# Kernel tuning notes

Measured on AMD Instinct MI355X. Metric: run time of the kernel, lower is better.

The kernel has to match this reference:

```python
import jax, jax.numpy as jnp
import numpy as np

BATCH, SEQ, D_IN, D_OUT = 32, 1024, 128, 128
NEG_SLOPE = 0.1


def setup_inputs() -> dict:
    key = jax.random.key(0)
    k1, k2, k3, k4 = jax.random.split(key, 4)
    nodes = jax.random.normal(k1, (BATCH, SEQ, D_IN), dtype=jnp.float32)
    adjacent = jax.random.randint(k2, (BATCH, SEQ, SEQ), 0, 2, dtype=jnp.int32)
    W = jax.random.normal(k3, (D_IN, D_OUT), dtype=jnp.float32) / np.sqrt(D_IN)
    B = jax.random.normal(k4, (D_IN, D_OUT), dtype=jnp.float32) / np.sqrt(D_IN)
    return {"nodes": nodes, "adjacent": adjacent, "W": W, "B": B}


def reference(nodes, adjacent, W, B):
    # mask[b, out, in] = 1 if edge (out -> in) present
    mask = (adjacent != 0).astype(nodes.dtype)
    # counts[b, in] = in-degree (number of 'out' neighbors pooled per target node)
    counts = mask.sum(axis=1)                               # [b, s_in]
    # segment-sum of neighbor features: pooled[b, in, d] = sum_out mask * nodes[b, out, d]
    pooled = jnp.einsum('boi,bod->bid', mask, nodes)        # [b, s_in, d]
    # mean over neighbors; nodes with zero degree get no pooled contribution
    pooled = jnp.where(counts[..., None] > 0,
                       pooled / jnp.maximum(counts, 1.0)[..., None],
                       jnp.zeros((), dtype=nodes.dtype))
    updated = nodes @ B + pooled @ W                        # [b, s, d_out]
    return jax.nn.leaky_relu(updated, negative_slope=NEG_SLOPE)
```

## Files before the change

kernel.cpp:

```cpp
#include <hip/hip_runtime.h>
#include <hip/hip_bf16.h>

#define SEQ 1024
#define DIM 128
#define NEG_SLOPE 0.1f

typedef __bf16 bf16x8 __attribute__((ext_vector_type(8)));
typedef float f32x4v __attribute__((ext_vector_type(4)));

#define BUF_STRIDE 24576
#define NODES_OFF  8192

__device__ __forceinline__ int swz(int row, int unit) {
    const int x  = row >> 2;
    const int fx = ((x & 3) | ((x & 1) << 2)) ^ ((x >> 2) & 7);
    return row * 128 + ((unit ^ fx) << 4);
}

__device__ __forceinline__ void bar() {
    asm volatile("s_waitcnt lgkmcnt(0)" ::: "memory");
    __builtin_amdgcn_s_barrier();
    __builtin_amdgcn_sched_barrier(0);
}

__device__ __forceinline__ unsigned short bfb(float f) {
    __bf16 h = (__bf16)f;
    return __builtin_bit_cast(unsigned short, h);
}
__device__ __forceinline__ unsigned mpack(int x0, int x1) {
    unsigned m0 = (x0 != 0) ? 0x3F80u : 0u;
    unsigned m1 = (x1 != 0) ? 0x3F80u : 0u;
    return m0 | (m1 << 16);
}

__global__ __launch_bounds__(256, 2)
void gcn_fused(const float* __restrict__ nodes,
               const int* __restrict__ adj,
               const float* __restrict__ W,
               const float* __restrict__ Bm,
               float* __restrict__ out)
{
    __shared__ alignas(16) unsigned char lds[2 * BUF_STRIDE];

    const int bid   = blockIdx.x;
    const int xcd   = bid & 7;
    const int slot  = bid >> 3;
    const int batch = ((slot >> 4) << 3) | xcd;
    const int mtile = slot & 15;
    const int i0    = mtile << 6;

    const int tid  = threadIdx.x;
    const int wave = tid >> 6;
    const int lane = tid & 63;
    const int wm   = wave >> 1;
    const int wn   = wave & 1;
    const int lrow = lane & 15;
    const int quad = lane >> 4;

    const int*   __restrict__ adj_b   = adj   + (size_t)batch * SEQ * SEQ;
    const float* __restrict__ nodes_b = nodes + (size_t)batch * SEQ * DIM;

    const int a_row = (tid >> 4) * 4;
    const int a_col = (tid & 15) * 4;
    const int n_row = (tid >> 5) * 4;
    const int n_col = (tid & 31) * 4;

    const int m_unit = (tid >> 4) >> 1;
    const int m_sub  = ((tid >> 4) & 1) * 8;
    const int n_unit = (tid >> 5) >> 1;
    const int n_sub  = ((tid >> 5) & 1) * 8;

    f32x4v acc[2][4] = {};
    f32x4v acc_cnt[2] = {};

    bf16x8 ones;
    #pragma unroll
    for (int j = 0; j < 8; ++j) ones[j] = __builtin_bit_cast(__bf16, (unsigned short)0x3F80);

    int4   A0[4], A1[4];
    float4 N0[8], N1[8];

    auto load_chunk = [&](int o0, int4 (&A)[4], float4 (&N)[8]) {
        const int* pa = adj_b + (size_t)(o0 + a_row) * SEQ + (i0 + a_col);
        #pragma unroll
        for (int r = 0; r < 4; ++r) A[r] = *(const int4*)(pa + (size_t)r * SEQ);
        const float* pn = nodes_b + (size_t)(o0 + n_row) * DIM + n_col;
        #pragma unroll
        for (int it = 0; it < 2; ++it)
            #pragma unroll
            for (int r = 0; r < 4; ++r)
                N[it * 4 + r] = *(const float4*)(pn + (size_t)(it * 32 + r) * DIM);
    };

    auto write_lds = [&](int base, const int4 (&A)[4], const float4 (&N)[8]) {
        unsigned char* mb = lds + base;
        unsigned char* nb = lds + base + NODES_OFF;
        #pragma unroll
        for (int j = 0; j < 4; ++j) {
            uint2 w;
            w.x = mpack(((const int*)&A[0])[j], ((const int*)&A[1])[j]);
            w.y = mpack(((const int*)&A[2])[j], ((const int*)&A[3])[j]);
            *(uint2*)(mb + swz(a_col + j, m_unit) + m_sub) = w;
        }
        #pragma unroll
        for (int it = 0; it < 2; ++it) {
            #pragma unroll
            for (int j = 0; j < 4; ++j) {
                uint2 w;
                w.x = (unsigned)bfb(((const float*)&N[it*4+0])[j]) |
                      ((unsigned)bfb(((const float*)&N[it*4+1])[j]) << 16);
                w.y = (unsigned)bfb(((const float*)&N[it*4+2])[j]) |
                      ((unsigned)bfb(((const float*)&N[it*4+3])[j]) << 16);
                *(uint2*)(nb + swz(n_col + j, 4 * it + n_unit) + n_sub) = w;
            }
        }
    };

    auto compute = [&](int base) {
        const unsigned char* mb = lds + base;
        const unsigned char* nb = lds + base + NODES_OFF;
        #pragma unroll
        for (int kk = 0; kk < 2; ++kk) {
            bf16x8 av[2], bv[4];
            av[0] = *(const bf16x8*)(mb + swz(wm * 32 +      lrow, 4 * kk + quad));
            av[1] = *(const bf16x8*)(mb + swz(wm * 32 + 16 + lrow, 4 * kk + quad));
            #pragma unroll
            for (int nf = 0; nf < 4; ++nf)
                bv[nf] = *(const bf16x8*)(nb + swz(wn * 64 + nf * 16 + lrow, 4 * kk + quad));
            #pragma unroll
            for (int mf = 0; mf < 2; ++mf) {
                #pragma unroll
                for (int nf = 0; nf < 4; ++nf)
                    acc[mf][nf] = __builtin_amdgcn_mfma_f32_16x16x32_bf16(av[mf], bv[nf], acc[mf][nf], 0, 0, 0);
                acc_cnt[mf] = __builtin_amdgcn_mfma_f32_16x16x32_bf16(av[mf], ones, acc_cnt[mf], 0, 0, 0);
            }
        }
    };

    load_chunk(0,   A0, N0);
    load_chunk(64,  A1, N1);
    write_lds(0, A0, N0);
    load_chunk(128, A0, N0);
    bar();

    for (int cc = 0; cc < 8; ++cc) {
        const int c0 = cc * 2;
        compute(0);
        write_lds(BUF_STRIDE, A1, N1);
        if (c0 + 3 < 16) load_chunk((c0 + 3) * 64, A1, N1);
        bar();
        compute(BUF_STRIDE);
        if (c0 + 2 < 16) write_lds(0, A0, N0);
        if (c0 + 4 < 16) load_chunk((c0 + 4) * 64, A0, N0);
        bar();
    }

    unsigned short (*pooled)[136] = (unsigned short (*)[136])(void*)lds;
    #pragma unroll
    for (int mf = 0; mf < 2; ++mf) {
        #pragma unroll
        for (int r = 0; r < 4; ++r) {
            const int row = wm * 32 + mf * 16 + quad * 4 + r;
            const float cnt = acc_cnt[mf][r];
            const float inv = (cnt > 0.5f) ? 1.0f / cnt : 0.0f;
            #pragma unroll
            for (int nf = 0; nf < 4; ++nf) {
                const int col = wn * 64 + nf * 16 + lrow;
                pooled[row][col] = bfb(acc[mf][nf][r] * inv);
            }
        }
    }
    __syncthreads();

    f32x4v acc2[2][4] = {};
    const int d_b0 = wn * 64 + lrow;

    #pragma unroll
    for (int ks = 0; ks < 4; ++ks) {
        const int k0 = ks * 32 + quad * 8;
        bf16x8 av[2];
        #pragma unroll
        for (int mf = 0; mf < 2; ++mf)
            av[mf] = *(const bf16x8*)&pooled[wm * 32 + mf * 16 + lrow][k0];
        bf16x8 bv[4];
        const float* pw = W + (size_t)k0 * DIM + d_b0;
        #pragma unroll
        for (int nf = 0; nf < 4; ++nf) {
            #pragma unroll
            for (int j = 0; j < 8; ++j)
                bv[nf][j] = (__bf16)pw[j * DIM + nf * 16];
        }
        #pragma unroll
        for (int mf = 0; mf < 2; ++mf)
            #pragma unroll
            for (int nf = 0; nf < 4; ++nf)
                acc2[mf][nf] = __builtin_amdgcn_mfma_f32_16x16x32_bf16(av[mf], bv[nf], acc2[mf][nf], 0, 0, 0);
    }

    #pragma unroll
    for (int ks = 0; ks < 4; ++ks) {
        const int k0 = ks * 32 + quad * 8;
        bf16x8 av[2];
        #pragma unroll
        for (int mf = 0; mf < 2; ++mf) {
            const float* p = nodes_b + (size_t)(i0 + wm * 32 + mf * 16 + lrow) * DIM + k0;
            const float4 f1 = *(const float4*)p;
            const float4 f2 = *(const float4*)(p + 4);
            av[mf][0] = (__bf16)f1.x; av[mf][1] = (__bf16)f1.y;
            av[mf][2] = (__bf16)f1.z; av[mf][3] = (__bf16)f1.w;
            av[mf][4] = (__bf16)f2.x; av[mf][5] = (__bf16)f2.y;
            av[mf][6] = (__bf16)f2.z; av[mf][7] = (__bf16)f2.w;
        }
        bf16x8 bv[4];
        const float* pB = Bm + (size_t)k0 * DIM + d_b0;
        #pragma unroll
        for (int nf = 0; nf < 4; ++nf) {
            #pragma unroll
            for (int j = 0; j < 8; ++j)
                bv[nf][j] = (__bf16)pB[j * DIM + nf * 16];
        }
        #pragma unroll
        for (int mf = 0; mf < 2; ++mf)
            #pragma unroll
            for (int nf = 0; nf < 4; ++nf)
                acc2[mf][nf] = __builtin_amdgcn_mfma_f32_16x16x32_bf16(av[mf], bv[nf], acc2[mf][nf], 0, 0, 0);
    }

    float* out_b = out + (size_t)batch * SEQ * DIM;
    #pragma unroll
    for (int mf = 0; mf < 2; ++mf) {
        #pragma unroll
        for (int nf = 0; nf < 4; ++nf) {
            const int col = wn * 64 + nf * 16 + lrow;
            #pragma unroll
            for (int r = 0; r < 4; ++r) {
                const int row = i0 + wm * 32 + mf * 16 + quad * 4 + r;
                const float x = acc2[mf][nf][r];
                out_b[(size_t)row * DIM + col] = (x > 0.0f) ? x : NEG_SLOPE * x;
            }
        }
    }
}

extern "C" void kernel_launch(void* const* d_in, const int* in_sizes, int n_in,
                              void* d_out, int out_size, void* d_ws, size_t ws_size,
                              hipStream_t stream) {
    const float* nodes = (const float*)d_in[0];
    const int*   adj   = (const int*)d_in[1];
    const float* W     = (const float*)d_in[2];
    const float* Bm    = (const float*)d_in[3];
    float*       out   = (float*)d_out;
    gcn_fused<<<dim3(512), dim3(256), 0, stream>>>(nodes, adj, W, Bm, out);
}
```

Before: 222.6 us.

## Double block size to 512 threads with 2x4 wave grid and halved per-thread loads

The block grows from 4 to 8 waves over the same 64-row tile. The 2x4 wave grid gives each wave 32 output columns instead of 64, and each thread loads half as much adjacency and node data per chunk. This doubles the number of waves in flight per block to hide the latency of the memory-bound adjacency stream, and lowers per-thread register use. In exchange the ones-MFMA count computation is now done redundantly by twice as many waves, and each block carries more barrier and sync overhead.

After: 228.5 us. 2.7% more time.

```diff
diff --git a/kernel.cpp b/kernel.cpp
--- a/kernel.cpp
+++ b/kernel.cpp
@@ -33,7 +33,7 @@
     return m0 | (m1 << 16);
 }
 
-__global__ __launch_bounds__(256, 2)
+__global__ __launch_bounds__(512, 4)
 void gcn_fused(const float* __restrict__ nodes,
                const int* __restrict__ adj,
                const float* __restrict__ W,
@@ -52,67 +52,58 @@
     const int tid  = threadIdx.x;
     const int wave = tid >> 6;
     const int lane = tid & 63;
-    const int wm   = wave >> 1;
-    const int wn   = wave & 1;
+    const int wm   = wave >> 2;
+    const int wn   = wave & 3;
     const int lrow = lane & 15;
     const int quad = lane >> 4;
 
     const int*   __restrict__ adj_b   = adj   + (size_t)batch * SEQ * SEQ;
     const float* __restrict__ nodes_b = nodes + (size_t)batch * SEQ * DIM;
 
-    const int a_row = (tid >> 4) * 4;
-    const int a_col = (tid & 15) * 4;
-    const int n_row = (tid >> 5) * 4;
-    const int n_col = (tid & 31) * 4;
-
-    const int m_unit = (tid >> 4) >> 1;
-    const int m_sub  = ((tid >> 4) & 1) * 8;
-    const int n_unit = (tid >> 5) >> 1;
-    const int n_sub  = ((tid >> 5) & 1) * 8;
-
-    f32x4v acc[2][4] = {};
+    const int sg     = tid >> 5;
+    const int o_off  = sg * 4;
+    const int a_col2 = (tid & 31) * 2;
+    const int n_col  = (tid & 31) * 4;
+    const int unit_s = sg >> 1;
+    const int sub_s  = (sg & 1) * 8;
+
+    f32x4v acc[2][2] = {};
     f32x4v acc_cnt[2] = {};
 
     bf16x8 ones;
     #pragma unroll
     for (int j = 0; j < 8; ++j) ones[j] = __builtin_bit_cast(__bf16, (unsigned short)0x3F80);
 
-    int4   A0[4], A1[4];
-    float4 N0[8], N1[8];
-
-    auto load_chunk = [&](int o0, int4 (&A)[4], float4 (&N)[8]) {
-        const int* pa = adj_b + (size_t)(o0 + a_row) * SEQ + (i0 + a_col);
-        #pragma unroll
-        for (int r = 0; r < 4; ++r) A[r] = *(const int4*)(pa + (size_t)r * SEQ);
-        const float* pn = nodes_b + (size_t)(o0 + n_row) * DIM + n_col;
-        #pragma unroll
-        for (int it = 0; it < 2; ++it)
-            #pragma unroll
-            for (int r = 0; r < 4; ++r)
-                N[it * 4 + r] = *(const float4*)(pn + (size_t)(it * 32 + r) * DIM);
+    int2   A0[4], A1[4];
+    float4 N0[4], N1[4];
+
+    auto load_chunk = [&](int o0, int2 (&A)[4], float4 (&N)[4]) {
+        const int* pa = adj_b + (size_t)(o0 + o_off) * SEQ + (i0 + a_col2);
+        #pragma unroll
+        for (int r = 0; r < 4; ++r) A[r] = *(const int2*)(pa + (size_t)r * SEQ);
+        const float* pn = nodes_b + (size_t)(o0 + o_off) * DIM + n_col;
+        #pragma unroll
+        for (int r = 0; r < 4; ++r) N[r] = *(const float4*)(pn + (size_t)r * DIM);
     };
 
-    auto write_lds = [&](int base, const int4 (&A)[4], const float4 (&N)[8]) {
+    auto write_lds = [&](int base, const int2 (&A)[4], const float4 (&N)[4]) {
         unsigned char* mb = lds + base;
         unsigned char* nb = lds + base + NODES_OFF;
         #pragma unroll
+        for (int j = 0; j < 2; ++j) {
+            uint2 w;
+            w.x = mpack(j ? A[0].y : A[0].x, j ? A[1].y : A[1].x);
+            w.y = mpack(j ? A[2].y : A[2].x, j ? A[3].y : A[3].x);
+            *(uint2*)(mb + swz(a_col2 + j, unit_s) + sub_s) = w;
+        }
+        #pragma unroll
         for (int j = 0; j < 4; ++j) {
             uint2 w;
-            w.x = mpack(((const int*)&A[0])[j], ((const int*)&A[1])[j]);
-            w.y = mpack(((const int*)&A[2])[j], ((const int*)&A[3])[j]);
-            *(uint2*)(mb + swz(a_col + j, m_unit) + m_sub) = w;
-        }
-        #pragma unroll
-        for (int it = 0; it < 2; ++it) {
-            #pragma unroll
-            for (int j = 0; j < 4; ++j) {
-                uint2 w;
-                w.x = (unsigned)bfb(((const float*)&N[it*4+0])[j]) |
-                      ((unsigned)bfb(((const float*)&N[it*4+1])[j]) << 16);
-                w.y = (unsigned)bfb(((const float*)&N[it*4+2])[j]) |
-                      ((unsigned)bfb(((const float*)&N[it*4+3])[j]) << 16);
-                *(uint2*)(nb + swz(n_col + j, 4 * it + n_unit) + n_sub) = w;
-            }
+            w.x = (unsigned)bfb(((const float*)&N[0])[j]) |
+                  ((unsigned)bfb(((const float*)&N[1])[j]) << 16);
+            w.y = (unsigned)bfb(((const float*)&N[2])[j]) |
+                  ((unsigned)bfb(((const float*)&N[3])[j]) << 16);
+            *(uint2*)(nb + swz(n_col + j, unit_s) + sub_s) = w;
         }
     };
 
@@ -121,16 +112,17 @@
         const unsigned char* nb = lds + base + NODES_OFF;
         #pragma unroll
         for (int kk = 0; kk < 2; ++kk) {
-            bf16x8 av[2], bv[4];
-            av[0] = *(const bf16x8*)(mb + swz(wm * 32 +      lrow, 4 * kk + quad));
-            av[1] = *(const bf16x8*)(mb + swz(wm * 32 + 16 + lrow, 4 * kk + quad));
-            #pragma unroll
-            for (int nf = 0; nf < 4; ++nf)
-                bv[nf] = *(const bf16x8*)(nb + swz(wn * 64 + nf * 16 + lrow, 4 * kk + quad));
+            bf16x8 av[2], bv[2];
+            #pragma unroll
+            for (int mf = 0; mf < 2; ++mf)
+                av[mf] = *(const bf16x8*)(mb + swz(wm * 32 + mf * 16 + lrow, 4 * kk + quad));
+            #pragma unroll
+            for (int nf = 0; nf < 2; ++nf)
+                bv[nf] = *(const bf16x8*)(nb + swz(wn * 32 + nf * 16 + lrow, 4 * kk + quad));
             #pragma unroll
             for (int mf = 0; mf < 2; ++mf) {
                 #pragma unroll
-                for (int nf = 0; nf < 4; ++nf)
+                for (int nf = 0; nf < 2; ++nf)
                     acc[mf][nf] = __builtin_amdgcn_mfma_f32_16x16x32_bf16(av[mf], bv[nf], acc[mf][nf], 0, 0, 0);
                 acc_cnt[mf] = __builtin_amdgcn_mfma_f32_16x16x32_bf16(av[mf], ones, acc_cnt[mf], 0, 0, 0);
             }
@@ -164,16 +156,16 @@
             const float cnt = acc_cnt[mf][r];
             const float inv = (cnt > 0.5f) ? 1.0f / cnt : 0.0f;
             #pragma unroll
-            for (int nf = 0; nf < 4; ++nf) {
-                const int col = wn * 64 + nf * 16 + lrow;
+            for (int nf = 0; nf < 2; ++nf) {
+                const int col = wn * 32 + nf * 16 + lrow;
                 pooled[row][col] = bfb(acc[mf][nf][r] * inv);
             }
         }
     }
     __syncthreads();
 
-    f32x4v acc2[2][4] = {};
-    const int d_b0 = wn * 64 + lrow;
+    f32x4v acc2[2][2] = {};
+    const int d_b0 = wn * 32 + lrow;
 
     #pragma unroll
     for (int ks = 0; ks < 4; ++ks) {
@@ -182,10 +174,10 @@
         #pragma unroll
         for (int mf = 0; mf < 2; ++mf)
             av[mf] = *(const bf16x8*)&pooled[wm * 32 + mf * 16 + lrow][k0];
-        bf16x8 bv[4];
+        bf16x8 bv[2];
         const float* pw = W + (size_t)k0 * DIM + d_b0;
         #pragma unroll
-        for (int nf = 0; nf < 4; ++nf) {
+        for (int nf = 0; nf < 2; ++nf) {
             #pragma unroll
             for (int j = 0; j < 8; ++j)
                 bv[nf][j] = (__bf16)pw[j * DIM + nf * 16];
@@ -193,7 +185,7 @@
         #pragma unroll
         for (int mf = 0; mf < 2; ++mf)
             #pragma unroll
-            for (int nf = 0; nf < 4; ++nf)
+            for (int nf = 0; nf < 2; ++nf)
                 acc2[mf][nf] = __builtin_amdgcn_mfma_f32_16x16x32_bf16(av[mf], bv[nf], acc2[mf][nf], 0, 0, 0);
     }
 
@@ -211,10 +203,10 @@
             av[mf][4] = (__bf16)f2.x; av[mf][5] = (__bf16)f2.y;
             av[mf][6] = (__bf16)f2.z; av[mf][7] = (__bf16)f2.w;
         }
-        bf16x8 bv[4];
+        bf16x8 bv[2];
         const float* pB = Bm + (size_t)k0 * DIM + d_b0;
         #pragma unroll
-        for (int nf = 0; nf < 4; ++nf) {
+        for (int nf = 0; nf < 2; ++nf) {
             #pragma unroll
             for (int j = 0; j < 8; ++j)
                 bv[nf][j] = (__bf16)pB[j * DIM + nf * 16];
@@ -222,7 +214,7 @@
         #pragma unroll
         for (int mf = 0; mf < 2; ++mf)
             #pragma unroll
-            for (int nf = 0; nf < 4; ++nf)
+            for (int nf = 0; nf < 2; ++nf)
                 acc2[mf][nf] = __builtin_amdgcn_mfma_f32_16x16x32_bf16(av[mf], bv[nf], acc2[mf][nf], 0, 0, 0);
     }
 
@@ -230,8 +222,8 @@
     #pragma unroll
     for (int mf = 0; mf < 2; ++mf) {
         #pragma unroll
-        for (int nf = 0; nf < 4; ++nf) {
-            const int col = wn * 64 + nf * 16 + lrow;
+        for (int nf = 0; nf < 2; ++nf) {
+            const int col = wn * 32 + nf * 16 + lrow;
             #pragma unroll
             for (int r = 0; r < 4; ++r) {
                 const int row = i0 + wm * 32 + mf * 16 + quad * 4 + r;
@@ -250,5 +242,5 @@
     const float* W     = (const float*)d_in[2];
     const float* Bm    = (const float*)d_in[3];
     float*       out   = (float*)d_out;
-    gcn_fused<<<dim3(512), dim3(256), 0, stream>>>(nodes, adj, W, Bm, out);
-}
+    gcn_fused<<<dim3(512), dim3(512), 0, stream>>>(nodes, adj, W, Bm, out);
+}
```

## Pre-transpose nodes and weights to bf16, halve the row tile, double the grid

Applied to the files above, without the earlier changes.

Adds two small pre-pass kernels. One converts W and B to transposed bf16 copies, and one writes a transposed bf16 copy of nodes into the workspace. The main kernel then loads the B operand straight from global memory into registers instead of staging it through LDS. The row tile drops from 64 to 32 rows, which doubles the grid to 1024 blocks, shrinks LDS to the mask buffers only, and raises occupancy to 4 blocks per CU. The cost is two extra launches plus an extra write and read of nodes in bf16. The original kernel is kept as a fallback when the workspace is too small.

Result: slower. 240.3 us (+8.0%).

```diff
diff --git a/kernel.cpp b/kernel.cpp
--- a/kernel.cpp
+++ b/kernel.cpp
@@ -8,78 +8,274 @@
 typedef __bf16 bf16x8 __attribute__((ext_vector_type(8)));
 typedef float f32x4v __attribute__((ext_vector_type(4)));
 
-#define BUF_STRIDE 24576
-#define NODES_OFF  8192
-
-__device__ __forceinline__ int swz(int row, int unit) {
-    const int x  = row >> 2;
-    const int fx = ((x & 3) | ((x & 1) << 2)) ^ ((x >> 2) & 7);
-    return row * 128 + ((unit ^ fx) << 4);
-}
-
+__device__ __forceinline__ unsigned short bfb(float f) {
+    __bf16 h = (__bf16)f;
+    return __builtin_bit_cast(unsigned short, h);
+}
+__device__ __forceinline__ unsigned mpack(int x0, int x1) {
+    unsigned m0 = (x0 != 0) ? 0x3F80u : 0u;
+    unsigned m1 = (x1 != 0) ? 0x3F80u : 0u;
+    return m0 | (m1 << 16);
+}
+__device__ __forceinline__ int fxv(int x) {
+    return ((x & 3) | ((x & 1) << 2)) ^ ((x >> 2) & 7);
+}
 __device__ __forceinline__ void bar() {
     asm volatile("s_waitcnt lgkmcnt(0)" ::: "memory");
     __builtin_amdgcn_s_barrier();
     __builtin_amdgcn_sched_barrier(0);
 }
 
-__device__ __forceinline__ unsigned short bfb(float f) {
-    __bf16 h = (__bf16)f;
-    return __builtin_bit_cast(unsigned short, h);
-}
-__device__ __forceinline__ unsigned mpack(int x0, int x1) {
-    unsigned m0 = (x0 != 0) ? 0x3F80u : 0u;
-    unsigned m1 = (x1 != 0) ? 0x3F80u : 0u;
-    return m0 | (m1 << 16);
-}
-
-__global__ __launch_bounds__(256, 2)
+__global__ __launch_bounds__(256)
+void wb_t(const float* __restrict__ W, const float* __restrict__ Bm,
+          unsigned short* __restrict__ WT, unsigned short* __restrict__ BT) {
+    const int gid = blockIdx.x * 256 + threadIdx.x;
+    const int n = gid >> 7, k = gid & 127;
+    WT[gid] = bfb(W[k * DIM + n]);
+    BT[gid] = bfb(Bm[k * DIM + n]);
+}
+
+__global__ __launch_bounds__(256)
+void nodes_t_kernel(const float* __restrict__ nodes, unsigned short* __restrict__ nodesT) {
+    const int b  = blockIdx.x >> 4;
+    const int o0 = (blockIdx.x & 15) << 6;
+    __shared__ unsigned short T[DIM][66];
+
+    const float* src = nodes + (size_t)b * SEQ * DIM;
+    const int t = threadIdx.x & 31;
+    const int g = threadIdx.x >> 5;
+
+    float4 v[8];
+    #pragma unroll
+    for (int r = 0; r < 8; ++r)
+        v[r] = *(const float4*)(src + (size_t)(o0 + g * 8 + r) * DIM + 4 * t);
+    #pragma unroll
+    for (int j = 0; j < 4; ++j) {
+        #pragma unroll
+        for (int p = 0; p < 4; ++p) {
+            unsigned w = (unsigned)bfb(((const float*)&v[2 * p])[j]) |
+                         ((unsigned)bfb(((const float*)&v[2 * p + 1])[j]) << 16);
+            *(unsigned*)((unsigned char*)&T[0][0] + (size_t)(4 * t + j) * 132 + (g * 8 + 2 * p) * 2) = w;
+        }
+    }
+    __syncthreads();
+    const int d = threadIdx.x >> 1, h = threadIdx.x & 1;
+    unsigned u[16];
+    #pragma unroll
+    for (int s = 0; s < 16; ++s)
+        u[s] = *(const unsigned*)((const unsigned char*)&T[0][0] + (size_t)d * 132 + h * 64 + s * 4);
+    unsigned short* dst = nodesT + (size_t)b * DIM * SEQ + (size_t)d * SEQ + o0 + h * 32;
+    #pragma unroll
+    for (int s = 0; s < 4; ++s) {
+        uint4 q = make_uint4(u[4 * s], u[4 * s + 1], u[4 * s + 2], u[4 * s + 3]);
+        *(uint4*)((unsigned char*)dst + s * 16) = q;
+    }
+}
+
+__global__ __launch_bounds__(256, 4)
 void gcn_fused(const float* __restrict__ nodes,
                const int* __restrict__ adj,
-               const float* __restrict__ W,
-               const float* __restrict__ Bm,
+               const unsigned short* __restrict__ nodesT,
+               const unsigned short* __restrict__ WT,
+               const unsigned short* __restrict__ BT,
                float* __restrict__ out)
 {
-    __shared__ alignas(16) unsigned char lds[2 * BUF_STRIDE];
+    __shared__ union {
+        unsigned char  m[2][4096];
+        unsigned short pooled[32][136];
+    } u;
 
     const int bid   = blockIdx.x;
     const int xcd   = bid & 7;
     const int slot  = bid >> 3;
-    const int batch = ((slot >> 4) << 3) | xcd;
-    const int mtile = slot & 15;
-    const int i0    = mtile << 6;
+    const int batch = ((slot >> 5) << 3) | xcd;
+    const int itile = slot & 31;
+    const int i0    = itile << 5;
 
     const int tid  = threadIdx.x;
     const int wave = tid >> 6;
     const int lane = tid & 63;
-    const int wm   = wave >> 1;
-    const int wn   = wave & 1;
     const int lrow = lane & 15;
     const int quad = lane >> 4;
 
-    const int*   __restrict__ adj_b   = adj   + (size_t)batch * SEQ * SEQ;
+    const int*            __restrict__ adj_b   = adj    + (size_t)batch * SEQ * SEQ;
+    const float*          __restrict__ nodes_b = nodes  + (size_t)batch * SEQ * DIM;
+    const unsigned short* __restrict__ nT_b    = nodesT + (size_t)batch * DIM * SEQ;
+
+    const int tq   = tid >> 3;
+    const int ic   = tid & 7;
+    const int fxic = fxv(ic);
+    const int gi0  = i0 + 4 * ic;
+    const int o0   = 2 * tq;
+
+    const int fx0 = fxv(lrow >> 2);
+    const int fx1 = fxv(4 + (lrow >> 2));
+
+    f32x4v acc[2][2] = {};
+    f32x4v acc_cnt[2] = {};
+    bf16x8 ones;
+    #pragma unroll
+    for (int j = 0; j < 8; ++j) ones[j] = __builtin_bit_cast(__bf16, (unsigned short)0x3F80);
+
+    int4   A0[2], A1[2];
+    bf16x8 bvA[4], bvB[4];
+
+    auto load_adj = [&](int c, int4 (&A)[2]) {
+        const int* pa = adj_b + (size_t)(c * 64 + o0) * SEQ + gi0;
+        A[0] = *(const int4*)pa;
+        A[1] = *(const int4*)(pa + SEQ);
+    };
+    auto load_bv = [&](int c, bf16x8 (&bv)[4]) {
+        const unsigned short* pn = nT_b + (size_t)(wave * 32 + lrow) * SEQ + c * 64 + quad * 8;
+        bv[0] = *(const bf16x8*)(pn);
+        bv[1] = *(const bf16x8*)(pn + 16 * SEQ);
+        bv[2] = *(const bf16x8*)(pn + 32);
+        bv[3] = *(const bf16x8*)(pn + 16 * SEQ + 32);
+    };
+    auto write_mask = [&](int b, const int4 (&A)[2]) {
+        unsigned char* mb = u.m[b];
+        #pragma unroll
+        for (int j = 0; j < 4; ++j) {
+            unsigned w = mpack(((const int*)&A[0])[j], ((const int*)&A[1])[j]);
+            *(unsigned*)(mb + (4 * ic + j) * 128 + (((tq >> 2) ^ fxic) << 4) + 4 * (tq & 3)) = w;
+        }
+    };
+    auto compute = [&](int b, const bf16x8 (&bv)[4]) {
+        const unsigned char* mb = u.m[b];
+        #pragma unroll
+        for (int kk = 0; kk < 2; ++kk) {
+            bf16x8 av0 = *(const bf16x8*)(mb + lrow * 128        + (((4 * kk + quad) ^ fx0) << 4));
+            bf16x8 av1 = *(const bf16x8*)(mb + (16 + lrow) * 128 + (((4 * kk + quad) ^ fx1) << 4));
+            acc[0][0] = __builtin_amdgcn_mfma_f32_16x16x32_bf16(av0, bv[2 * kk + 0], acc[0][0], 0, 0, 0);
+            acc[0][1] = __builtin_amdgcn_mfma_f32_16x16x32_bf16(av0, bv[2 * kk + 1], acc[0][1], 0, 0, 0);
+            acc[1][0] = __builtin_amdgcn_mfma_f32_16x16x32_bf16(av1, bv[2 * kk + 0], acc[1][0], 0, 0, 0);
+            acc[1][1] = __builtin_amdgcn_mfma_f32_16x16x32_bf16(av1, bv[2 * kk + 1], acc[1][1], 0, 0, 0);
+            acc_cnt[0] = __builtin_amdgcn_mfma_f32_16x16x32_bf16(av0, ones, acc_cnt[0], 0, 0, 0);
+            acc_cnt[1] = __builtin_amdgcn_mfma_f32_16x16x32_bf16(av1, ones, acc_cnt[1], 0, 0, 0);
+        }
+    };
+
+    load_adj(0, A0); load_adj(1, A1);
+    load_bv(0, bvA); load_bv(1, bvB);
+    write_mask(0, A0);
+    load_adj(2, A0);
+    bar();
+
+    for (int cc = 0; cc < 8; ++cc) {
+        const int c0 = 2 * cc;
+        compute(0, bvA);
+        write_mask(1, A1);
+        if (c0 + 3 < 16) load_adj(c0 + 3, A1);
+        if (c0 + 2 < 16) load_bv(c0 + 2, bvA);
+        bar();
+        compute(1, bvB);
+        if (c0 + 2 < 16) write_mask(0, A0);
+        if (c0 + 4 < 16) load_adj(c0 + 4, A0);
+        if (c0 + 3 < 16) load_bv(c0 + 3, bvB);
+        bar();
+    }
+
+    #pragma unroll
+    for (int mf = 0; mf < 2; ++mf) {
+        #pragma unroll
+        for (int r = 0; r < 4; ++r) {
+            const int row = mf * 16 + quad * 4 + r;
+            const float cnt = acc_cnt[mf][r];
+            const float inv = (cnt > 0.5f) ? 1.0f / cnt : 0.0f;
+            #pragma unroll
+            for (int nf = 0; nf < 2; ++nf)
+                u.pooled[row][wave * 32 + nf * 16 + lrow] = bfb(acc[mf][nf][r] * inv);
+        }
+    }
+    bar();
+
+    f32x4v acc2[2][2] = {};
+    const int dn = wave * 32 + lrow;
+
+    #pragma unroll
+    for (int ks = 0; ks < 4; ++ks) {
+        const int k0 = ks * 32 + quad * 8;
+        bf16x8 av[2], bv2[2];
+        #pragma unroll
+        for (int mf = 0; mf < 2; ++mf)
+            av[mf] = *(const bf16x8*)((const unsigned char*)&u.pooled[0][0] + (mf * 16 + lrow) * 272 + k0 * 2);
+        #pragma unroll
+        for (int nf = 0; nf < 2; ++nf)
+            bv2[nf] = *(const bf16x8*)(WT + (size_t)(dn + nf * 16) * DIM + k0);
+        #pragma unroll
+        for (int mf = 0; mf < 2; ++mf)
+            #pragma unroll
+            for (int nf = 0; nf < 2; ++nf)
+                acc2[mf][nf] = __builtin_amdgcn_mfma_f32_16x16x32_bf16(av[mf], bv2[nf], acc2[mf][nf], 0, 0, 0);
+    }
+    #pragma unroll
+    for (int ks = 0; ks < 4; ++ks) {
+        const int k0 = ks * 32 + quad * 8;
+        bf16x8 av[2], bv2[2];
+        #pragma unroll
+        for (int mf = 0; mf < 2; ++mf) {
+            const float* p = nodes_b + (size_t)(i0 + mf * 16 + lrow) * DIM + k0;
+            const float4 f1 = *(const float4*)p;
+            const float4 f2 = *(const float4*)(p + 4);
+            av[mf][0] = (__bf16)f1.x; av[mf][1] = (__bf16)f1.y;
+            av[mf][2] = (__bf16)f1.z; av[mf][3] = (__bf16)f1.w;
+            av[mf][4] = (__bf16)f2.x; av[mf][5] = (__bf16)f2.y;
+            av[mf][6] = (__bf16)f2.z; av[mf][7] = (__bf16)f2.w;
+        }
+        #pragma unroll
+        for (int nf = 0; nf < 2; ++nf)
+            bv2[nf] = *(const bf16x8*)(BT + (size_t)(dn + nf * 16) * DIM + k0);
+        #pragma unroll
+        for (int mf = 0; mf < 2; ++mf)
+            #pragma unroll
+            for (int nf = 0; nf < 2; ++nf)
+                acc2[mf][nf] = __builtin_amdgcn_mfma_f32_16x16x32_bf16(av[mf], bv2[nf], acc2[mf][nf], 0, 0, 0);
+    }
+
+    float* out_b = out + (size_t)batch * SEQ * DIM;
+    #pragma unroll
+    for (int mf = 0; mf < 2; ++mf) {
+        #pragma unroll
+        for (int nf = 0; nf < 2; ++nf) {
+            const int col = wave * 32 + nf * 16 + lrow;
+            #pragma unroll
+            for (int r = 0; r < 4; ++r) {
+                const int row = i0 + mf * 16 + quad * 4 + r;
+                const float x = acc2[mf][nf][r];
+                out_b[(size_t)row * DIM + col] = (x > 0.0f) ? x : NEG_SLOPE * x;
+            }
+        }
+    }
+}
+
+#define BUF_STRIDE 24576
+#define NODES_OFF  8192
+__device__ __forceinline__ int fb_swz(int row, int unit) {
+    const int x  = row >> 2;
+    const int fx = ((x & 3) | ((x & 1) << 2)) ^ ((x >> 2) & 7);
+    return row * 128 + ((unit ^ fx) << 4);
+}
+__global__ __launch_bounds__(256, 2)
+void gcn_fused_fb(const float* __restrict__ nodes, const int* __restrict__ adj,
+                  const float* __restrict__ W, const float* __restrict__ Bm,
+                  float* __restrict__ out)
+{
+    __shared__ alignas(16) unsigned char lds[2 * BUF_STRIDE];
+    const int bid = blockIdx.x, xcd = bid & 7, slot = bid >> 3;
+    const int batch = ((slot >> 4) << 3) | xcd, mtile = slot & 15, i0 = mtile << 6;
+    const int tid = threadIdx.x, wave = tid >> 6, lane = tid & 63;
+    const int wm = wave >> 1, wn = wave & 1, lrow = lane & 15, quad = lane >> 4;
+    const int* __restrict__ adj_b = adj + (size_t)batch * SEQ * SEQ;
     const float* __restrict__ nodes_b = nodes + (size_t)batch * SEQ * DIM;
-
-    const int a_row = (tid >> 4) * 4;
-    const int a_col = (tid & 15) * 4;
-    const int n_row = (tid >> 5) * 4;
-    const int n_col = (tid & 31) * 4;
-
-    const int m_unit = (tid >> 4) >> 1;
-    const int m_sub  = ((tid >> 4) & 1) * 8;
-    const int n_unit = (tid >> 5) >> 1;
-    const int n_sub  = ((tid >> 5) & 1) * 8;
-
-    f32x4v acc[2][4] = {};
-    f32x4v acc_cnt[2] = {};
-
+    const int a_row = (tid >> 4) * 4, a_col = (tid & 15) * 4;
+    const int n_row = (tid >> 5) * 4, n_col = (tid & 31) * 4;
+    const int m_unit = (tid >> 4) >> 1, m_sub = ((tid >> 4) & 1) * 8;
+    const int n_unit = (tid >> 5) >> 1, n_sub = ((tid >> 5) & 1) * 8;
+    f32x4v acc[2][4] = {}; f32x4v acc_cnt[2] = {};
     bf16x8 ones;
     #pragma unroll
     for (int j = 0; j < 8; ++j) ones[j] = __builtin_bit_cast(__bf16, (unsigned short)0x3F80);
-
-    int4   A0[4], A1[4];
-    float4 N0[8], N1[8];
-
+    int4 A0[4], A1[4]; float4 N0[8], N1[8];
     auto load_chunk = [&](int o0, int4 (&A)[4], float4 (&N)[8]) {
         const int* pa = adj_b + (size_t)(o0 + a_row) * SEQ + (i0 + a_col);
         #pragma unroll
@@ -91,42 +287,36 @@
             for (int r = 0; r < 4; ++r)
                 N[it * 4 + r] = *(const float4*)(pn + (size_t)(it * 32 + r) * DIM);
     };
-
     auto write_lds = [&](int base, const int4 (&A)[4], const float4 (&N)[8]) {
-        unsigned char* mb = lds + base;
-        unsigned char* nb = lds + base + NODES_OFF;
+        unsigned char* mb = lds + base; unsigned char* nb = lds + base + NODES_OFF;
         #pragma unroll
         for (int j = 0; j < 4; ++j) {
             uint2 w;
             w.x = mpack(((const int*)&A[0])[j], ((const int*)&A[1])[j]);
             w.y = mpack(((const int*)&A[2])[j], ((const int*)&A[3])[j]);
-            *(uint2*)(mb + swz(a_col + j, m_unit) + m_sub) = w;
+            *(uint2*)(mb + fb_swz(a_col + j, m_unit) + m_sub) = w;
         }
         #pragma unroll
         for (int it = 0; it < 2; ++it) {
             #pragma unroll
             for (int j = 0; j < 4; ++j) {
                 uint2 w;
-                w.x = (unsigned)bfb(((const float*)&N[it*4+0])[j]) |
-                      ((unsigned)bfb(((const float*)&N[it*4+1])[j]) << 16);
-                w.y = (unsigned)bfb(((const float*)&N[it*4+2])[j]) |
-                      ((unsigned)bfb(((const float*)&N[it*4+3])[j]) << 16);
-                *(uint2*)(nb + swz(n_col + j, 4 * it + n_unit) + n_sub) = w;
+                w.x = (unsigned)bfb(((const float*)&N[it*4+0])[j]) | ((unsigned)bfb(((const float*)&N[it*4+1])[j]) << 16);
+                w.y = (unsigned)bfb(((const float*)&N[it*4+2])[j]) | ((unsigned)bfb(((const float*)&N[it*4+3])[j]) << 16);
+                *(uint2*)(nb + fb_swz(n_col + j, 4 * it + n_unit) + n_sub) = w;
             }
         }
     };
-
     auto compute = [&](int base) {
-        const unsigned char* mb = lds + base;
-        const unsigned char* nb = lds + base + NODES_OFF;
+        const unsigned char* mb = lds + base; const unsigned char* nb = lds + base + NODES_OFF;
         #pragma unroll
         for (int kk = 0; kk < 2; ++kk) {
             bf16x8 av[2], bv[4];
-            av[0] = *(const bf16x8*)(mb + swz(wm * 32 +      lrow, 4 * kk + quad));
-            av[1] = *(const bf16x8*)(mb + swz(wm * 32 + 16 + lrow, 4 * kk + quad));
+            av[0] = *(const bf16x8*)(mb + fb_swz(wm * 32 + lrow, 4 * kk + quad));
+            av[1] = *(const bf16x8*)(mb + fb_swz(wm * 32 + 16 + lrow, 4 * kk + quad));
             #pragma unroll
             for (int nf = 0; nf < 4; ++nf)
-                bv[nf] = *(const bf16x8*)(nb + swz(wn * 64 + nf * 16 + lrow, 4 * kk + quad));
+                bv[nf] = *(const bf16x8*)(nb + fb_swz(wn * 64 + nf * 16 + lrow, 4 * kk + quad));
             #pragma unroll
             for (int mf = 0; mf < 2; ++mf) {
                 #pragma unroll
@@ -136,17 +326,11 @@
             }
         }
     };
-
-    load_chunk(0,   A0, N0);
-    load_chunk(64,  A1, N1);
-    write_lds(0, A0, N0);
-    load_chunk(128, A0, N0);
-    bar();
-
+    load_chunk(0, A0, N0); load_chunk(64, A1, N1);
+    write_lds(0, A0, N0); load_chunk(128, A0, N0); bar();
     for (int cc = 0; cc < 8; ++cc) {
         const int c0 = cc * 2;
-        compute(0);
-        write_lds(BUF_STRIDE, A1, N1);
+        compute(0); write_lds(BUF_STRIDE, A1, N1);
         if (c0 + 3 < 16) load_chunk((c0 + 3) * 64, A1, N1);
         bar();
         compute(BUF_STRIDE);
@@ -154,27 +338,21 @@
         if (c0 + 4 < 16) load_chunk((c0 + 4) * 64, A0, N0);
         bar();
     }
-
     unsigned short (*pooled)[136] = (unsigned short (*)[136])(void*)lds;
     #pragma unroll
-    for (int mf = 0; mf < 2; ++mf) {
+    for (int mf = 0; mf < 2; ++mf)
         #pragma unroll
         for (int r = 0; r < 4; ++r) {
             const int row = wm * 32 + mf * 16 + quad * 4 + r;
             const float cnt = acc_cnt[mf][r];
             const float inv = (cnt > 0.5f) ? 1.0f / cnt : 0.0f;
             #pragma unroll
-            for (int nf = 0; nf < 4; ++nf) {
-                const int col = wn * 64 + nf * 16 + lrow;
-                pooled[row][col] = bfb(acc[mf][nf][r] * inv);
-            }
-        }
-    }
+            for (int nf = 0; nf < 4; ++nf)
+                pooled[row][wn * 64 + nf * 16 + lrow] = bfb(acc[mf][nf][r] * inv);
+        }
     __syncthreads();
-
     f32x4v acc2[2][4] = {};
     const int d_b0 = wn * 64 + lrow;
-
     #pragma unroll
     for (int ks = 0; ks < 4; ++ks) {
         const int k0 = ks * 32 + quad * 8;
@@ -185,18 +363,15 @@
         bf16x8 bv[4];
         const float* pw = W + (size_t)k0 * DIM + d_b0;
         #pragma unroll
-        for (int nf = 0; nf < 4; ++nf) {
-            #pragma unroll
-            for (int j = 0; j < 8; ++j)
-                bv[nf][j] = (__bf16)pw[j * DIM + nf * 16];
-        }
+        for (int nf = 0; nf < 4; ++nf)
+            #pragma unroll
+            for (int j = 0; j < 8; ++j) bv[nf][j] = (__bf16)pw[j * DIM + nf * 16];
         #pragma unroll
         for (int mf = 0; mf < 2; ++mf)
             #pragma unroll
             for (int nf = 0; nf < 4; ++nf)
                 acc2[mf][nf] = __builtin_amdgcn_mfma_f32_16x16x32_bf16(av[mf], bv[nf], acc2[mf][nf], 0, 0, 0);
     }
-
     #pragma unroll
     for (int ks = 0; ks < 4; ++ks) {
         const int k0 = ks * 32 + quad * 8;
@@ -204,8 +379,7 @@
         #pragma unroll
         for (int mf = 0; mf < 2; ++mf) {
             const float* p = nodes_b + (size_t)(i0 + wm * 32 + mf * 16 + lrow) * DIM + k0;
-            const float4 f1 = *(const float4*)p;
-            const float4 f2 = *(const float4*)(p + 4);
+            const float4 f1 = *(const float4*)p; const float4 f2 = *(const float4*)(p + 4);
             av[mf][0] = (__bf16)f1.x; av[mf][1] = (__bf16)f1.y;
             av[mf][2] = (__bf16)f1.z; av[mf][3] = (__bf16)f1.w;
             av[mf][4] = (__bf16)f2.x; av[mf][5] = (__bf16)f2.y;
@@ -214,21 +388,18 @@
         bf16x8 bv[4];
         const float* pB = Bm + (size_t)k0 * DIM + d_b0;
         #pragma unroll
-        for (int nf = 0; nf < 4; ++nf) {
-            #pragma unroll
-            for (int j = 0; j < 8; ++j)
-                bv[nf][j] = (__bf16)pB[j * DIM + nf * 16];
-        }
+        for (int nf = 0; nf < 4; ++nf)
+            #pragma unroll
+            for (int j = 0; j < 8; ++j) bv[nf][j] = (__bf16)pB[j * DIM + nf * 16];
         #pragma unroll
         for (int mf = 0; mf < 2; ++mf)
             #pragma unroll
             for (int nf = 0; nf < 4; ++nf)
                 acc2[mf][nf] = __builtin_amdgcn_mfma_f32_16x16x32_bf16(av[mf], bv[nf], acc2[mf][nf], 0, 0, 0);
     }
-
     float* out_b = out + (size_t)batch * SEQ * DIM;
     #pragma unroll
-    for (int mf = 0; mf < 2; ++mf) {
+    for (int mf = 0; mf < 2; ++mf)
         #pragma unroll
         for (int nf = 0; nf < 4; ++nf) {
             const int col = wn * 64 + nf * 16 + lrow;
@@ -239,7 +410,6 @@
                 out_b[(size_t)row * DIM + col] = (x > 0.0f) ? x : NEG_SLOPE * x;
             }
         }
-    }
 }
 
 extern "C" void kernel_launch(void* const* d_in, const int* in_sizes, int n_in,
@@ -250,5 +420,19 @@
     const float* W     = (const float*)d_in[2];
     const float* Bm    = (const float*)d_in[3];
     float*       out   = (float*)d_out;
-    gcn_fused<<<dim3(512), dim3(256), 0, stream>>>(nodes, adj, W, Bm, out);
-}
+
+    const size_t NT_BYTES = (size_t)32 * DIM * SEQ * 2;
+    const size_t WB_BYTES = (size_t)DIM * DIM * 2;
+    const size_t NEED = NT_BYTES + 2 * WB_BYTES;
+
+    if (d_ws != nullptr && ws_size >= NEED) {
+        unsigned short* nodesT = (unsigned short*)d_ws;
+        unsigned short* WT = (unsigned short*)((char*)d_ws + NT_BYTES);
+        unsigned short* BT = (unsigned short*)((char*)d_ws + NT_BYTES + WB_BYTES);
+        wb_t<<<dim3(64), dim3(256), 0, stream>>>(W, Bm, WT, BT);
+        nodes_t_kernel<<<dim3(512), dim3(256), 0, stream>>>(nodes, nodesT);
+        gcn_fused<<<dim3(1024), dim3(256), 0, stream>>>(nodes, adj, nodesT, WT, BT, out);
+    } else {
+        gcn_fused_fb<<<dim3(512), dim3(256), 0, stream>>>(nodes, adj, W, Bm, out);
+    }
+}
```

## Double output-row tile to 128 per block with 512 threads

Applied to the files above, without the earlier changes.

Each block now covers 128 target rows instead of 64, using 8 waves and 256 blocks. Every streamed chunk of node features is therefore shared by twice as many output rows, roughly halving redundant global reads of the nodes tensor. The adjacency and node loads are re-mapped so each thread handles one 4x4 piece, and the LDS buffers are enlarged to match. The trade-off is a larger LDS footprint per block and only one block per CU on a 256-block grid, which may reduce latency hiding.

Result: no change. 219.5 us (-1.4%).

```diff
diff --git a/kernel.cpp b/kernel.cpp
--- a/kernel.cpp
+++ b/kernel.cpp
@@ -8,21 +8,20 @@
 typedef __bf16 bf16x8 __attribute__((ext_vector_type(8)));
 typedef float f32x4v __attribute__((ext_vector_type(4)));
 
-#define BUF_STRIDE 24576
-#define NODES_OFF  8192
-
+#define BUF_STRIDE 32768
+#define NODES_OFF  16384
+
+__device__ __forceinline__ int fxv(int x) {
+    return ((x & 3) | ((x & 1) << 2)) ^ ((x >> 2) & 7);
+}
 __device__ __forceinline__ int swz(int row, int unit) {
-    const int x  = row >> 2;
-    const int fx = ((x & 3) | ((x & 1) << 2)) ^ ((x >> 2) & 7);
-    return row * 128 + ((unit ^ fx) << 4);
-}
-
+    return row * 128 + ((unit ^ fxv(row >> 2)) << 4);
+}
 __device__ __forceinline__ void bar() {
     asm volatile("s_waitcnt lgkmcnt(0)" ::: "memory");
     __builtin_amdgcn_s_barrier();
     __builtin_amdgcn_sched_barrier(0);
 }
-
 __device__ __forceinline__ unsigned short bfb(float f) {
     __bf16 h = (__bf16)f;
     return __builtin_bit_cast(unsigned short, h);
@@ -33,7 +32,7 @@
     return m0 | (m1 << 16);
 }
 
-__global__ __launch_bounds__(256, 2)
+__global__ __launch_bounds__(512, 2)
 void gcn_fused(const float* __restrict__ nodes,
                const int* __restrict__ adj,
                const float* __restrict__ W,
@@ -45,9 +44,9 @@
     const int bid   = blockIdx.x;
     const int xcd   = bid & 7;
     const int slot  = bid >> 3;
-    const int batch = ((slot >> 4) << 3) | xcd;
-    const int mtile = slot & 15;
-    const int i0    = mtile << 6;
+    const int batch = ((slot >> 3) << 3) | xcd;
+    const int itile = slot & 7;
+    const int i0    = itile << 7;
 
     const int tid  = threadIdx.x;
     const int wave = tid >> 6;
@@ -60,39 +59,32 @@
     const int*   __restrict__ adj_b   = adj   + (size_t)batch * SEQ * SEQ;
     const float* __restrict__ nodes_b = nodes + (size_t)batch * SEQ * DIM;
 
-    const int a_row = (tid >> 4) * 4;
-    const int a_col = (tid & 15) * 4;
+    const int a_row = (tid >> 5) * 4;
+    const int a_col = (tid & 31) * 4;
     const int n_row = (tid >> 5) * 4;
     const int n_col = (tid & 31) * 4;
-
-    const int m_unit = (tid >> 4) >> 1;
-    const int m_sub  = ((tid >> 4) & 1) * 8;
-    const int n_unit = (tid >> 5) >> 1;
-    const int n_sub  = ((tid >> 5) & 1) * 8;
+    const int unit_s = (tid >> 5) >> 1;
+    const int sub_s  = ((tid >> 5) & 1) * 8;
 
     f32x4v acc[2][4] = {};
     f32x4v acc_cnt[2] = {};
-
     bf16x8 ones;
     #pragma unroll
     for (int j = 0; j < 8; ++j) ones[j] = __builtin_bit_cast(__bf16, (unsigned short)0x3F80);
 
     int4   A0[4], A1[4];
-    float4 N0[8], N1[8];
-
-    auto load_chunk = [&](int o0, int4 (&A)[4], float4 (&N)[8]) {
+    float4 N0[4], N1[4];
+
+    auto load_chunk = [&](int o0, int4 (&A)[4], float4 (&N)[4]) {
         const int* pa = adj_b + (size_t)(o0 + a_row) * SEQ + (i0 + a_col);
         #pragma unroll
         for (int r = 0; r < 4; ++r) A[r] = *(const int4*)(pa + (size_t)r * SEQ);
         const float* pn = nodes_b + (size_t)(o0 + n_row) * DIM + n_col;
         #pragma unroll
-        for (int it = 0; it < 2; ++it)
-            #pragma unroll
-            for (int r = 0; r < 4; ++r)
-                N[it * 4 + r] = *(const float4*)(pn + (size_t)(it * 32 + r) * DIM);
+        for (int r = 0; r < 4; ++r) N[r] = *(const float4*)(pn + (size_t)r * DIM);
     };
 
-    auto write_lds = [&](int base, const int4 (&A)[4], const float4 (&N)[8]) {
+    auto write_lds = [&](int base, const int4 (&A)[4], const float4 (&N)[4]) {
         unsigned char* mb = lds + base;
         unsigned char* nb = lds + base + NODES_OFF;
         #pragma unroll
@@ -100,19 +92,16 @@
             uint2 w;
             w.x = mpack(((const int*)&A[0])[j], ((const int*)&A[1])[j]);
             w.y = mpack(((const int*)&A[2])[j], ((const int*)&A[3])[j]);
-            *(uint2*)(mb + swz(a_col + j, m_unit) + m_sub) = w;
-        }
-        #pragma unroll
-        for (int it = 0; it < 2; ++it) {
-            #pragma unroll
-            for (int j = 0; j < 4; ++j) {
-                uint2 w;
-                w.x = (unsigned)bfb(((const float*)&N[it*4+0])[j]) |
-                      ((unsigned)bfb(((const float*)&N[it*4+1])[j]) << 16);
-                w.y = (unsigned)bfb(((const float*)&N[it*4+2])[j]) |
-                      ((unsigned)bfb(((const float*)&N[it*4+3])[j]) << 16);
-                *(uint2*)(nb + swz(n_col + j, 4 * it + n_unit) + n_sub) = w;
-            }
+            *(uint2*)(mb + swz(a_col + j, unit_s) + sub_s) = w;
+        }
+        #pragma unroll
+        for (int j = 0; j < 4; ++j) {
+            uint2 w;
+            w.x = (unsigned)bfb(((const float*)&N[0])[j]) |
+                  ((unsigned)bfb(((const float*)&N[1])[j]) << 16);
+            w.y = (unsigned)bfb(((const float*)&N[2])[j]) |
+                  ((unsigned)bfb(((const float*)&N[3])[j]) << 16);
+            *(uint2*)(nb + swz(n_col + j, unit_s) + sub_s) = w;
         }
     };
 
@@ -122,8 +111,9 @@
         #pragma unroll
         for (int kk = 0; kk < 2; ++kk) {
             bf16x8 av[2], bv[4];
-            av[0] = *(const bf16x8*)(mb + swz(wm * 32 +      lrow, 4 * kk + quad));
-            av[1] = *(const bf16x8*)(mb + swz(wm * 32 + 16 + lrow, 4 * kk + quad));
+            #pragma unroll
+            for (int mf = 0; mf < 2; ++mf)
+                av[mf] = *(const bf16x8*)(mb + swz(wm * 32 + mf * 16 + lrow, 4 * kk + quad));
             #pragma unroll
             for (int nf = 0; nf < 4; ++nf)
                 bv[nf] = *(const bf16x8*)(nb + swz(wn * 64 + nf * 16 + lrow, 4 * kk + quad));
@@ -170,7 +160,7 @@
             }
         }
     }
-    __syncthreads();
+    bar();
 
     f32x4v acc2[2][4] = {};
     const int d_b0 = wn * 64 + lrow;
@@ -196,7 +186,6 @@
             for (int nf = 0; nf < 4; ++nf)
                 acc2[mf][nf] = __builtin_amdgcn_mfma_f32_16x16x32_bf16(av[mf], bv[nf], acc2[mf][nf], 0, 0, 0);
     }
-
     #pragma unroll
     for (int ks = 0; ks < 4; ++ks) {
         const int k0 = ks * 32 + quad * 8;
@@ -250,5 +239,5 @@
     const float* W     = (const float*)d_in[2];
     const float* Bm    = (const float*)d_in[3];
     float*       out   = (float*)d_out;
-    gcn_fused<<<dim3(512), dim3(256), 0, stream>>>(nodes, adj, W, Bm, out);
-}
+    gcn_fused<<<dim3(256), dim3(512), 0, stream>>>(nodes, adj, W, Bm, out);
+}
```
